# Optimization experiments

Measured on AMD Instinct MI355X. Metric: run time of the kernel, lower is better.

The kernel has to match this reference:

```python
import jax, jax.numpy as jnp
import numpy as np

D_MODEL = 1024
N_HEADS = 16
D_K = D_MODEL // N_HEADS


def setup_inputs() -> dict:
    key = jax.random.key(0)
    ks = jax.random.split(key, 11)
    B, S = 2, 2048
    scale = 0.02
    inp = {
        "q": jax.random.normal(ks[0], (B, S, D_MODEL), jnp.float32),
        "k": jax.random.normal(ks[1], (B, S, D_MODEL), jnp.float32),
        "v": jax.random.normal(ks[2], (B, S, D_MODEL), jnp.float32),
        "w_q": jax.random.normal(ks[3], (D_MODEL, D_MODEL), jnp.float32) * scale,
        "b_q": jnp.zeros((D_MODEL,), jnp.float32),
        "w_k": jax.random.normal(ks[4], (D_MODEL, D_MODEL), jnp.float32) * scale,
        "b_k": jnp.zeros((D_MODEL,), jnp.float32),
        "w_v": jax.random.normal(ks[5], (D_MODEL, D_MODEL), jnp.float32) * scale,
        "b_v": jnp.zeros((D_MODEL,), jnp.float32),
        "w_o": jax.random.normal(ks[6], (D_MODEL, D_MODEL), jnp.float32) * scale,
        "b_o": jnp.zeros((D_MODEL,), jnp.float32),
    }
    return inp


def reference(q, k, v, w_q, b_q, w_k, b_k, w_v, b_v, w_o, b_o):
    B, S, _ = q.shape
    # projections (torch Linear: x @ W.T + b); split into heads -> [B, H, S, d]
    def proj(x, w, b):
        return (x @ w.T + b).reshape(B, S, N_HEADS, D_K).transpose(0, 2, 1, 3)
    qh = proj(q, w_q, b_q)
    kh = proj(k, w_k, b_k)
    vh = proj(v, w_v, b_v)
    scores = jnp.einsum("bhqd,bhkd->bhqk", qh, kh) / jnp.sqrt(
        jnp.asarray(D_K, jnp.float32))
    attn = jax.nn.softmax(scores, axis=-1)  # dropout = identity (eval)
    out = jnp.einsum("bhqk,bhkd->bhqd", attn, vh)
    out = out.transpose(0, 2, 1, 3).reshape(B, S, D_MODEL)
    return out @ w_o.T + b_o
```

## Files before the change

kernel.cpp:

```cpp
#include <hip/hip_runtime.h>

typedef unsigned short u16;
typedef unsigned int u32;
typedef __attribute__((ext_vector_type(4))) unsigned short u16x4;
typedef __attribute__((ext_vector_type(8))) unsigned short u16x8;
typedef __attribute__((ext_vector_type(8))) __bf16 bf16x8;
typedef __attribute__((ext_vector_type(4))) float f32x4;

#define SEQ 2048
#define DMODEL 1024
#define LDP 3072
#define MM (DMODEL * DMODEL)

__device__ __forceinline__ u16 f2bf(float f) {
  unsigned u = __builtin_bit_cast(unsigned, f);
  u = (u + 0x7fffu + ((u >> 16) & 1u)) >> 16;
  return (u16)u;
}

__device__ __forceinline__ u32 cvtpk(float lo, float hi) {
  u32 r;
  asm volatile("v_cvt_pk_bf16_f32 %0, %1, %2" : "=v"(r) : "v"(lo), "v"(hi));
  return r;
}

__device__ __forceinline__ float fexp2(float x) {
#if __has_builtin(__builtin_amdgcn_exp2f)
  return __builtin_amdgcn_exp2f(x);
#else
  return exp2f(x);
#endif
}

__device__ __forceinline__ bf16x8 ldbf8(const u16* p) {
  return __builtin_bit_cast(bf16x8, *(const u16x8*)p);
}
__device__ __forceinline__ bf16x8 ldbf8c(const char* p) {
  return __builtin_bit_cast(bf16x8, *(const u16x8*)p);
}

__device__ __forceinline__ f32x4 mfma16(bf16x8 a, bf16x8 b, f32x4 c) {
  return __builtin_amdgcn_mfma_f32_16x16x32_bf16(a, b, c, 0, 0, 0);
}

__device__ __forceinline__ void gl16(const void* g, void* l) {
  __builtin_amdgcn_global_load_lds(
      (__attribute__((address_space(1))) void*)(size_t)g,
      (__attribute__((address_space(3))) void*)l, 16, 0, 0);
}

__device__ __forceinline__ void cast8(const float* __restrict__ s, u16* __restrict__ d) {
  const size_t i = ((size_t)blockIdx.x * blockDim.x + threadIdx.x) * 8;
  const float4 a = *(const float4*)(s + i);
  const float4 b = *(const float4*)(s + i + 4);
  u16x8 o;
  o[0] = f2bf(a.x); o[1] = f2bf(a.y); o[2] = f2bf(a.z); o[3] = f2bf(a.w);
  o[4] = f2bf(b.x); o[5] = f2bf(b.y); o[6] = f2bf(b.z); o[7] = f2bf(b.w);
  *(u16x8*)(d + i) = o;
}

__global__ void cast_qkv_k(const float* __restrict__ q, const float* __restrict__ k,
                           const float* __restrict__ v, u16* __restrict__ dq,
                           u16* __restrict__ dk, u16* __restrict__ dv) {
  const int z = blockIdx.y;
  cast8(z == 0 ? q : z == 1 ? k : v, z == 0 ? dq : z == 1 ? dk : dv);
}

__global__ void cast_w_k(const float* __restrict__ wq, const float* __restrict__ wk,
                         const float* __restrict__ wv, const float* __restrict__ wo,
                         u16* __restrict__ wqkv, u16* __restrict__ wob) {
  const int z = blockIdx.y;
  const float* s = z == 0 ? wq : z == 1 ? wk : z == 2 ? wv : wo;
  u16* d = z < 3 ? wqkv + (size_t)z * MM : wob;
  cast8(s, d);
}

template <int OMODE>
__device__ __forceinline__ void gemm_bt_body(const u16* __restrict__ A,
                                             const u16* __restrict__ Bw,
                                             const float* __restrict__ bias,
                                             void* __restrict__ Cv, const int K,
                                             const int ldc, const int ncol0,
                                             const int m0, const int n0) {
  __shared__ u16 As[128 * 32];
  __shared__ u16 Bs[128 * 32];
  const int tid = threadIdx.x;
  const int lane = tid & 63;
  const int w = tid >> 6;
  const int l15 = lane & 15;
  const int lg = lane >> 4;

  f32x4 acc[4][4] = {};

  const int arow = (w >> 1) * 64 + l15;
  const int brow = (w & 1) * 64 + l15;
  const int kfb = lg * 16;

  const int strow = w * 32 + (lane >> 2);
  const u16* Ag = A + (size_t)(m0 + strow) * K + (lane & 3) * 8;
  const u16* Bg = Bw + (size_t)(n0 + strow) * K + (lane & 3) * 8;
  const size_t rstep = (size_t)16 * K;
  char* AsL0 = (char*)As + w * 32 * 64;
  char* AsL1 = AsL0 + 16 * 64;
  char* BsL0 = (char*)Bs + w * 32 * 64;
  char* BsL1 = BsL0 + 16 * 64;

  for (int k0 = 0; k0 < K; k0 += 32) {
    __syncthreads();
    gl16(Ag + k0, AsL0);
    gl16(Ag + k0 + rstep, AsL1);
    gl16(Bg + k0, BsL0);
    gl16(Bg + k0 + rstep, BsL1);
    __syncthreads();
    bf16x8 af[4], bfv[4];
#pragma unroll
    for (int t = 0; t < 4; ++t) {
      af[t] = ldbf8c((char*)As + (arow + t * 16) * 64 + kfb);
      bfv[t] = ldbf8c((char*)Bs + (brow + t * 16) * 64 + kfb);
    }
    __builtin_amdgcn_s_setprio(1);
#pragma unroll
    for (int i = 0; i < 4; ++i)
#pragma unroll
      for (int j = 0; j < 4; ++j) acc[i][j] = mfma16(af[i], bfv[j], acc[i][j]);
    __builtin_amdgcn_s_setprio(0);
  }

  const int mrow = (w >> 1) * 64 + lg * 4;
  const int ncol = (w & 1) * 64 + l15;
#pragma unroll
  for (int j = 0; j < 4; ++j) {
    const int gn = n0 + ncol + j * 16;
    const float bia = bias[gn];
#pragma unroll
    for (int i = 0; i < 4; ++i) {
      const int gmb = m0 + mrow + i * 16;
#pragma unroll
      for (int r = 0; r < 4; ++r) {
        const float val = acc[i][j][r] + bia;
        const int gm = gmb + r;
        if (OMODE == 0) {
          ((float*)Cv)[(size_t)gm * ldc + gn] = val;
        } else if (OMODE == 1) {
          ((u16*)Cv)[(size_t)gm * ldc + ncol0 + gn] = f2bf(val);
        } else {
          const int bb = gm >> 11, ss = gm & 2047;
          const int hh = gn >> 6, dd = gn & 63;
          ((u16*)Cv)[(((size_t)(bb * 16 + hh) * 64 + dd) << 11) + ss] = f2bf(val);
        }
      }
    }
  }
}

__global__ __launch_bounds__(256, 3) void gemm_qkv_k(
    const u16* __restrict__ qb, const u16* __restrict__ kb,
    const u16* __restrict__ vb, const u16* __restrict__ wqkv,
    const float* __restrict__ bq, const float* __restrict__ bk,
    const float* __restrict__ bv, u16* __restrict__ proj, u16* __restrict__ vtb) {
  const int b = blockIdx.x;
  const int xcd = b & 7;
  const int i = b >> 3;
  const int z = i >> 5;
  const int j = i & 31;
  const int m0 = (xcd * 4 + (j >> 3)) * 128;
  const int n0 = (j & 7) * 128;
  if (z == 2)
    gemm_bt_body<2>(vb, wqkv + 2 * (size_t)MM, bv, vtb, DMODEL, 0, 0, m0, n0);
  else
    gemm_bt_body<1>(z == 0 ? qb : kb, wqkv + (size_t)z * MM, z == 0 ? bq : bk,
                    proj, DMODEL, LDP, z * DMODEL, m0, n0);
}

__global__ __launch_bounds__(256, 3) void gemm_o_k(const u16* __restrict__ attnb,
                                                   const u16* __restrict__ wob,
                                                   const float* __restrict__ bo,
                                                   float* __restrict__ out) {
  const int b = blockIdx.x;
  const int xcd = b & 7;
  const int i = b >> 3;
  const int m0 = (xcd * 4 + (i >> 3)) * 128;
  const int n0 = (i & 7) * 128;
  gemm_bt_body<0>(attnb, wob, bo, out, DMODEL, DMODEL, 0, m0, n0);
}

__global__ __launch_bounds__(256, 4) void attn_k(const u16* __restrict__ proj,
                                                 const u16* __restrict__ vtb,
                                                 u16* __restrict__ outa) {
  __shared__ u16 ks[2][64 * 64];
  __shared__ u16 vs[2][64 * 64];
  const int b = blockIdx.x;
  const int slot = b >> 3;
  const int bh = (b & 7) * 4 + (slot >> 5);
  const int qB = (slot & 31) * 64;
  const int tid = threadIdx.x;
  const int lane = tid & 63;
  const int w = tid >> 6;
  const size_t rb = (size_t)(bh >> 4) * SEQ;
  const int h = bh & 15;
  const int l15 = lane & 15;
  const int lg = lane >> 4;
  const int sw = (l15 & 7) << 4;
  const int c0 = (lg * 16) ^ sw;
  const int c1 = (lg * 16 + 64) ^ sw;
  const int rowb = l15 * 128;

  const u16* qp = proj + (rb + qB + w * 16 + l15) * LDP + h * 64 + lg * 8;
  const bf16x8 qf0 = ldbf8(qp);
  const bf16x8 qf1 = ldbf8(qp + 32);

  const int srow = tid >> 2;
  const int scel = (tid & 3) * 16;
  const int stz0 = srow * 128 + (((tid & 3) * 32) ^ ((srow & 7) << 4));
  const int stz1 = srow * 128 + ((((tid & 3) * 32) + 16) ^ ((srow & 7) << 4));
  const u16* kg = proj + rb * LDP + DMODEL + h * 64;
  const u16* vg = vtb + (size_t)bh * 64 * SEQ;

  u16x8 ka0, ka1, va0, va1;
  {
    const u16* kr = kg + (size_t)srow * LDP + scel;
    ka0 = *(const u16x8*)kr;
    ka1 = *(const u16x8*)(kr + 8);
    const u16* vr = vg + (size_t)srow * SEQ + scel;
    va0 = *(const u16x8*)vr;
    va1 = *(const u16x8*)(vr + 8);
  }

  f32x4 oacc[4] = {};
  float mrun = -3.0e38f, lrun = 0.f;
  int p = 0;

  for (int kv0 = 0; kv0 < SEQ; kv0 += 64) {
    {
      char* kd = (char*)ks[p];
      char* vd = (char*)vs[p];
      *(u16x8*)(kd + stz0) = ka0;
      *(u16x8*)(kd + stz1) = ka1;
      *(u16x8*)(vd + stz0) = va0;
      *(u16x8*)(vd + stz1) = va1;
    }
    __syncthreads();
    if (kv0 + 64 < SEQ) {
      const u16* kr = kg + (size_t)(kv0 + 64 + srow) * LDP + scel;
      ka0 = *(const u16x8*)kr;
      ka1 = *(const u16x8*)(kr + 8);
      const u16* vr = vg + (size_t)srow * SEQ + kv0 + 64 + scel;
      va0 = *(const u16x8*)vr;
      va1 = *(const u16x8*)(vr + 8);
    }
    const char* kb = (const char*)ks[p];
    f32x4 st[4];
    __builtin_amdgcn_s_setprio(1);
#pragma unroll
    for (int t = 0; t < 4; ++t) {
      const bf16x8 k0 = ldbf8c(kb + t * 2048 + rowb + c0);
      const bf16x8 k1 = ldbf8c(kb + t * 2048 + rowb + c1);
      f32x4 s = {};
      s = mfma16(k0, qf0, s);
      s = mfma16(k1, qf1, s);
      st[t] = s * 0.18033688f;
    }
    __builtin_amdgcn_s_setprio(0);

    float mx0 = fmaxf(fmaxf(st[0][0], st[0][1]), fmaxf(st[0][2], st[0][3]));
    float mx1 = fmaxf(fmaxf(st[1][0], st[1][1]), fmaxf(st[1][2], st[1][3]));
    float mx2 = fmaxf(fmaxf(st[2][0], st[2][1]), fmaxf(st[2][2], st[2][3]));
    float mx3 = fmaxf(fmaxf(st[3][0], st[3][1]), fmaxf(st[3][2], st[3][3]));
    float mx = fmaxf(fmaxf(mx0, mx1), fmaxf(mx2, mx3));
    mx = fmaxf(mx, __shfl_xor(mx, 16));
    mx = fmaxf(mx, __shfl_xor(mx, 32));
    if (!__all(mx <= mrun + 11.5416f)) {
      const float mn = fmaxf(mrun, mx);
      const float sf = fexp2(mrun - mn);
      mrun = mn;
      lrun *= sf;
#pragma unroll
      for (int t = 0; t < 4; ++t)
#pragma unroll
        for (int r = 0; r < 4; ++r) oacc[t][r] *= sf;
    }
    float rs = 0.f;
    u32 pku[4][2];
#pragma unroll
    for (int t = 0; t < 4; ++t) {
      const float e0 = fexp2(st[t][0] - mrun);
      const float e1 = fexp2(st[t][1] - mrun);
      const float e2 = fexp2(st[t][2] - mrun);
      const float e3 = fexp2(st[t][3] - mrun);
      rs += (e0 + e1) + (e2 + e3);
      pku[t][0] = cvtpk(e0, e1);
      pku[t][1] = cvtpk(e2, e3);
    }
    rs += __shfl_xor(rs, 16);
    rs += __shfl_xor(rs, 32);
    lrun += rs;

    u16x8 pb0, pb1;
    ((u32*)&pb0)[0] = pku[0][0]; ((u32*)&pb0)[1] = pku[0][1];
    ((u32*)&pb0)[2] = pku[1][0]; ((u32*)&pb0)[3] = pku[1][1];
    ((u32*)&pb1)[0] = pku[2][0]; ((u32*)&pb1)[1] = pku[2][1];
    ((u32*)&pb1)[2] = pku[3][0]; ((u32*)&pb1)[3] = pku[3][1];
    const bf16x8 pf0 = __builtin_bit_cast(bf16x8, pb0);
    const bf16x8 pf1 = __builtin_bit_cast(bf16x8, pb1);

    const char* vbp = (const char*)vs[p];
    const int vo0 = (8 * lg) ^ sw;
    __builtin_amdgcn_s_setprio(1);
#pragma unroll
    for (int dt = 0; dt < 4; ++dt) {
      const char* vrow = vbp + (dt * 16 + l15) * 128;
      u16x8 vf0, vf1;
      *(u16x4*)&vf0       = *(const u16x4*)(vrow + vo0);
      *((u16x4*)&vf0 + 1) = *(const u16x4*)(vrow + (vo0 ^ 32));
      *(u16x4*)&vf1       = *(const u16x4*)(vrow + (vo0 ^ 64));
      *((u16x4*)&vf1 + 1) = *(const u16x4*)(vrow + (vo0 ^ 96));
      oacc[dt] = mfma16(__builtin_bit_cast(bf16x8, vf0), pf0, oacc[dt]);
      oacc[dt] = mfma16(__builtin_bit_cast(bf16x8, vf1), pf1, oacc[dt]);
    }
    __builtin_amdgcn_s_setprio(0);
    p ^= 1;
  }

  const float invl = 1.0f / lrun;
  u16* orow = outa + (rb + qB + w * 16 + l15) * DMODEL + h * 64;
#pragma unroll
  for (int t = 0; t < 4; ++t) {
    const u32 p01 = cvtpk(oacc[t][0] * invl, oacc[t][1] * invl);
    const u32 p23 = cvtpk(oacc[t][2] * invl, oacc[t][3] * invl);
    *(u32*)((char*)orow + (t * 16 + lg * 4) * 2) = p01;
    *(u32*)((char*)orow + (t * 16 + lg * 4 + 2) * 2) = p23;
  }
}

extern "C" void kernel_launch(void* const* d_in, const int* in_sizes, int n_in,
                              void* d_out, int out_size, void* d_ws, size_t ws_size,
                              hipStream_t stream) {
  const float* q  = (const float*)d_in[0];
  const float* k  = (const float*)d_in[1];
  const float* v  = (const float*)d_in[2];
  const float* wq = (const float*)d_in[3];
  const float* bq = (const float*)d_in[4];
  const float* wk = (const float*)d_in[5];
  const float* bk = (const float*)d_in[6];
  const float* wv = (const float*)d_in[7];
  const float* bv = (const float*)d_in[8];
  const float* wo = (const float*)d_in[9];
  const float* bo = (const float*)d_in[10];

  const size_t NTOK = (size_t)2 * SEQ;
  const size_t NELE = NTOK * DMODEL;
  u16* qb    = (u16*)d_ws;
  u16* kb    = qb + NELE;
  u16* vb    = kb + NELE;
  u16* wqkv  = vb + NELE;
  u16* wob   = wqkv + 3 * (size_t)MM;
  u16* projb = wob + (size_t)MM;
  u16* vtb   = projb + NTOK * LDP;
  u16* attnb = qb;

  cast_qkv_k<<<dim3(2048, 3), 256, 0, stream>>>(q, k, v, qb, kb, vb);
  cast_w_k<<<dim3(512, 4), 256, 0, stream>>>(wq, wk, wv, wo, wqkv, wob);
  gemm_qkv_k<<<768, 256, 0, stream>>>(qb, kb, vb, wqkv, bq, bk, bv, projb, vtb);
  attn_k<<<1024, 256, 0, stream>>>(projb, vtb, attnb);
  gemm_o_k<<<256, 256, 0, stream>>>(attnb, wob, bo, (float*)d_out);
}
```

Before: 141.7 us.

## Switch attention to 32x32x16 MFMA with 128-query tiles per block

The attention kernel now has each wave handle 32 query rows with 32x32x16 bf16 MFMAs instead of 16 rows with 16x16x32. Each block covers 128 queries, which halves the grid and halves K/V LDS staging traffic per query. The softmax scale is folded into an FMA inside exp2, and the rescale threshold is adjusted to match unscaled scores. The trade is more accumulator registers (launch bounds drop from 4 to 2 blocks per CU) and fewer blocks, which lowers occupancy and parallelism.

After: 127.3 us. -10.1%, faster.

```diff
diff --git a/kernel.cpp b/kernel.cpp
--- a/kernel.cpp
+++ b/kernel.cpp
@@ -6,11 +6,13 @@
 typedef __attribute__((ext_vector_type(8))) unsigned short u16x8;
 typedef __attribute__((ext_vector_type(8))) __bf16 bf16x8;
 typedef __attribute__((ext_vector_type(4))) float f32x4;
+typedef __attribute__((ext_vector_type(16))) float f32x16;
 
 #define SEQ 2048
 #define DMODEL 1024
 #define LDP 3072
 #define MM (DMODEL * DMODEL)
+#define SC 0.18033688f
 
 __device__ __forceinline__ u16 f2bf(float f) {
   unsigned u = __builtin_bit_cast(unsigned, f);
@@ -41,6 +43,9 @@
 
 __device__ __forceinline__ f32x4 mfma16(bf16x8 a, bf16x8 b, f32x4 c) {
   return __builtin_amdgcn_mfma_f32_16x16x32_bf16(a, b, c, 0, 0, 0);
+}
+__device__ __forceinline__ f32x16 mfma32(bf16x8 a, bf16x8 b, f32x16 c) {
+  return __builtin_amdgcn_mfma_f32_32x32x16_bf16(a, b, c, 0, 0, 0);
 }
 
 __device__ __forceinline__ void gl16(const void* g, void* l) {
@@ -184,30 +189,28 @@
   gemm_bt_body<0>(attnb, wob, bo, out, DMODEL, DMODEL, 0, m0, n0);
 }
 
-__global__ __launch_bounds__(256, 4) void attn_k(const u16* __restrict__ proj,
+__global__ __launch_bounds__(256, 2) void attn_k(const u16* __restrict__ proj,
                                                  const u16* __restrict__ vtb,
                                                  u16* __restrict__ outa) {
   __shared__ u16 ks[2][64 * 64];
   __shared__ u16 vs[2][64 * 64];
   const int b = blockIdx.x;
   const int slot = b >> 3;
-  const int bh = (b & 7) * 4 + (slot >> 5);
-  const int qB = (slot & 31) * 64;
+  const int bh = (b & 7) * 4 + (slot >> 4);
+  const int qB = (slot & 15) * 128;
   const int tid = threadIdx.x;
   const int lane = tid & 63;
   const int w = tid >> 6;
   const size_t rb = (size_t)(bh >> 4) * SEQ;
   const int h = bh & 15;
-  const int l15 = lane & 15;
-  const int lg = lane >> 4;
-  const int sw = (l15 & 7) << 4;
-  const int c0 = (lg * 16) ^ sw;
-  const int c1 = (lg * 16 + 64) ^ sw;
-  const int rowb = l15 * 128;
-
-  const u16* qp = proj + (rb + qB + w * 16 + l15) * LDP + h * 64 + lg * 8;
-  const bf16x8 qf0 = ldbf8(qp);
-  const bf16x8 qf1 = ldbf8(qp + 32);
+  const int l31 = lane & 31;
+  const int hi = lane >> 5;
+  const int swz = (l31 & 7) << 4;
+
+  const u16* qp = proj + (rb + qB + w * 32 + l31) * LDP + h * 64 + hi * 8;
+  bf16x8 qf[4];
+#pragma unroll
+  for (int km = 0; km < 4; ++km) qf[km] = ldbf8(qp + km * 16);
 
   const int srow = tid >> 2;
   const int scel = (tid & 3) * 16;
@@ -226,7 +229,7 @@
     va1 = *(const u16x8*)(vr + 8);
   }
 
-  f32x4 oacc[4] = {};
+  f32x16 oa0 = {}, oa1 = {};
   float mrun = -3.0e38f, lrun = 0.f;
   int p = 0;
 
@@ -248,87 +251,96 @@
       va0 = *(const u16x8*)vr;
       va1 = *(const u16x8*)(vr + 8);
     }
-    const char* kb = (const char*)ks[p];
-    f32x4 st[4];
+    const char* kp = (const char*)ks[p];
+    const char* vp = (const char*)vs[p];
+    f32x16 s0 = {}, s1 = {};
     __builtin_amdgcn_s_setprio(1);
 #pragma unroll
-    for (int t = 0; t < 4; ++t) {
-      const bf16x8 k0 = ldbf8c(kb + t * 2048 + rowb + c0);
-      const bf16x8 k1 = ldbf8c(kb + t * 2048 + rowb + c1);
-      f32x4 s = {};
-      s = mfma16(k0, qf0, s);
-      s = mfma16(k1, qf1, s);
-      st[t] = s * 0.18033688f;
+    for (int km = 0; km < 4; ++km) {
+      const int co = (km * 32 + hi * 16) ^ swz;
+      const bf16x8 k0 = ldbf8c(kp + l31 * 128 + co);
+      const bf16x8 k1 = ldbf8c(kp + (32 + l31) * 128 + co);
+      s0 = mfma32(k0, qf[km], s0);
+      s1 = mfma32(k1, qf[km], s1);
     }
     __builtin_amdgcn_s_setprio(0);
 
-    float mx0 = fmaxf(fmaxf(st[0][0], st[0][1]), fmaxf(st[0][2], st[0][3]));
-    float mx1 = fmaxf(fmaxf(st[1][0], st[1][1]), fmaxf(st[1][2], st[1][3]));
-    float mx2 = fmaxf(fmaxf(st[2][0], st[2][1]), fmaxf(st[2][2], st[2][3]));
-    float mx3 = fmaxf(fmaxf(st[3][0], st[3][1]), fmaxf(st[3][2], st[3][3]));
-    float mx = fmaxf(fmaxf(mx0, mx1), fmaxf(mx2, mx3));
-    mx = fmaxf(mx, __shfl_xor(mx, 16));
+    float mxq0 = fmaxf(fmaxf(s0[0], s0[1]), fmaxf(s0[2], s0[3]));
+    float mxq1 = fmaxf(fmaxf(s0[4], s0[5]), fmaxf(s0[6], s0[7]));
+    float mxq2 = fmaxf(fmaxf(s0[8], s0[9]), fmaxf(s0[10], s0[11]));
+    float mxq3 = fmaxf(fmaxf(s0[12], s0[13]), fmaxf(s0[14], s0[15]));
+    float mxq4 = fmaxf(fmaxf(s1[0], s1[1]), fmaxf(s1[2], s1[3]));
+    float mxq5 = fmaxf(fmaxf(s1[4], s1[5]), fmaxf(s1[6], s1[7]));
+    float mxq6 = fmaxf(fmaxf(s1[8], s1[9]), fmaxf(s1[10], s1[11]));
+    float mxq7 = fmaxf(fmaxf(s1[12], s1[13]), fmaxf(s1[14], s1[15]));
+    float mx = fmaxf(fmaxf(fmaxf(mxq0, mxq1), fmaxf(mxq2, mxq3)),
+                     fmaxf(fmaxf(mxq4, mxq5), fmaxf(mxq6, mxq7)));
     mx = fmaxf(mx, __shfl_xor(mx, 32));
-    if (!__all(mx <= mrun + 11.5416f)) {
+    if (!__all(mx <= mrun + 64.0f)) {
       const float mn = fmaxf(mrun, mx);
-      const float sf = fexp2(mrun - mn);
+      const float sf = fexp2((mrun - mn) * SC);
       mrun = mn;
       lrun *= sf;
 #pragma unroll
-      for (int t = 0; t < 4; ++t)
-#pragma unroll
-        for (int r = 0; r < 4; ++r) oacc[t][r] *= sf;
-    }
-    float rs = 0.f;
-    u32 pku[4][2];
-#pragma unroll
-    for (int t = 0; t < 4; ++t) {
-      const float e0 = fexp2(st[t][0] - mrun);
-      const float e1 = fexp2(st[t][1] - mrun);
-      const float e2 = fexp2(st[t][2] - mrun);
-      const float e3 = fexp2(st[t][3] - mrun);
-      rs += (e0 + e1) + (e2 + e3);
-      pku[t][0] = cvtpk(e0, e1);
-      pku[t][1] = cvtpk(e2, e3);
-    }
-    rs += __shfl_xor(rs, 16);
+      for (int r = 0; r < 16; ++r) { oa0[r] *= sf; oa1[r] *= sf; }
+    }
+    const float nmc = -mrun * SC;
+#pragma unroll
+    for (int r = 0; r < 16; ++r) s0[r] = fexp2(__builtin_fmaf(s0[r], SC, nmc));
+#pragma unroll
+    for (int r = 0; r < 16; ++r) s1[r] = fexp2(__builtin_fmaf(s1[r], SC, nmc));
+    float rs = (((s0[0] + s0[1]) + (s0[2] + s0[3])) +
+                ((s0[4] + s0[5]) + (s0[6] + s0[7]))) +
+               (((s0[8] + s0[9]) + (s0[10] + s0[11])) +
+                ((s0[12] + s0[13]) + (s0[14] + s0[15])));
+    rs += (((s1[0] + s1[1]) + (s1[2] + s1[3])) +
+           ((s1[4] + s1[5]) + (s1[6] + s1[7]))) +
+          (((s1[8] + s1[9]) + (s1[10] + s1[11])) +
+           ((s1[12] + s1[13]) + (s1[14] + s1[15])));
     rs += __shfl_xor(rs, 32);
     lrun += rs;
 
-    u16x8 pb0, pb1;
-    ((u32*)&pb0)[0] = pku[0][0]; ((u32*)&pb0)[1] = pku[0][1];
-    ((u32*)&pb0)[2] = pku[1][0]; ((u32*)&pb0)[3] = pku[1][1];
-    ((u32*)&pb1)[0] = pku[2][0]; ((u32*)&pb1)[1] = pku[2][1];
-    ((u32*)&pb1)[2] = pku[3][0]; ((u32*)&pb1)[3] = pku[3][1];
-    const bf16x8 pf0 = __builtin_bit_cast(bf16x8, pb0);
-    const bf16x8 pf1 = __builtin_bit_cast(bf16x8, pb1);
-
-    const char* vbp = (const char*)vs[p];
-    const int vo0 = (8 * lg) ^ sw;
     __builtin_amdgcn_s_setprio(1);
-#pragma unroll
-    for (int dt = 0; dt < 4; ++dt) {
-      const char* vrow = vbp + (dt * 16 + l15) * 128;
-      u16x8 vf0, vf1;
-      *(u16x4*)&vf0       = *(const u16x4*)(vrow + vo0);
-      *((u16x4*)&vf0 + 1) = *(const u16x4*)(vrow + (vo0 ^ 32));
-      *(u16x4*)&vf1       = *(const u16x4*)(vrow + (vo0 ^ 64));
-      *((u16x4*)&vf1 + 1) = *(const u16x4*)(vrow + (vo0 ^ 96));
-      oacc[dt] = mfma16(__builtin_bit_cast(bf16x8, vf0), pf0, oacc[dt]);
-      oacc[dt] = mfma16(__builtin_bit_cast(bf16x8, vf1), pf1, oacc[dt]);
-    }
+#define PCHUNK(SV, G, CB)                                                \
+    {                                                                    \
+      u16x8 pbu;                                                         \
+      ((u32*)&pbu)[0] = cvtpk(SV[G + 0], SV[G + 1]);                     \
+      ((u32*)&pbu)[1] = cvtpk(SV[G + 2], SV[G + 3]);                     \
+      ((u32*)&pbu)[2] = cvtpk(SV[G + 4], SV[G + 5]);                     \
+      ((u32*)&pbu)[3] = cvtpk(SV[G + 6], SV[G + 7]);                     \
+      const bf16x8 pb = __builtin_bit_cast(bf16x8, pbu);                 \
+      const int vc0 = (CB + 8 * hi) ^ swz;                               \
+      const int vc1 = (CB + 16 + 8 * hi) ^ swz;                          \
+      const char* vr0 = vp + l31 * 128;                                  \
+      const char* vr1 = vp + (32 + l31) * 128;                           \
+      u16x8 vf0, vf1;                                                    \
+      *(u16x4*)&vf0       = *(const u16x4*)(vr0 + vc0);                  \
+      *((u16x4*)&vf0 + 1) = *(const u16x4*)(vr0 + vc1);                  \
+      *(u16x4*)&vf1       = *(const u16x4*)(vr1 + vc0);                  \
+      *((u16x4*)&vf1 + 1) = *(const u16x4*)(vr1 + vc1);                  \
+      oa0 = mfma32(__builtin_bit_cast(bf16x8, vf0), pb, oa0);            \
+      oa1 = mfma32(__builtin_bit_cast(bf16x8, vf1), pb, oa1);            \
+    }
+    PCHUNK(s0, 0, 0)
+    PCHUNK(s0, 8, 32)
+    PCHUNK(s1, 0, 64)
+    PCHUNK(s1, 8, 96)
+#undef PCHUNK
     __builtin_amdgcn_s_setprio(0);
     p ^= 1;
   }
 
   const float invl = 1.0f / lrun;
-  u16* orow = outa + (rb + qB + w * 16 + l15) * DMODEL + h * 64;
-#pragma unroll
-  for (int t = 0; t < 4; ++t) {
-    const u32 p01 = cvtpk(oacc[t][0] * invl, oacc[t][1] * invl);
-    const u32 p23 = cvtpk(oacc[t][2] * invl, oacc[t][3] * invl);
-    *(u32*)((char*)orow + (t * 16 + lg * 4) * 2) = p01;
-    *(u32*)((char*)orow + (t * 16 + lg * 4 + 2) * 2) = p23;
+  u16* orow = outa + (rb + qB + w * 32 + l31) * DMODEL + h * 64 + hi * 4;
+#pragma unroll
+  for (int g = 0; g < 4; ++g) {
+    u16x4 st0, st1;
+    ((u32*)&st0)[0] = cvtpk(oa0[4 * g + 0] * invl, oa0[4 * g + 1] * invl);
+    ((u32*)&st0)[1] = cvtpk(oa0[4 * g + 2] * invl, oa0[4 * g + 3] * invl);
+    *(u16x4*)(orow + 8 * g) = st0;
+    ((u32*)&st1)[0] = cvtpk(oa1[4 * g + 0] * invl, oa1[4 * g + 1] * invl);
+    ((u32*)&st1)[1] = cvtpk(oa1[4 * g + 2] * invl, oa1[4 * g + 3] * invl);
+    *(u16x4*)(orow + 32 + 8 * g) = st1;
   }
 }
 
@@ -361,6 +373,6 @@
   cast_qkv_k<<<dim3(2048, 3), 256, 0, stream>>>(q, k, v, qb, kb, vb);
   cast_w_k<<<dim3(512, 4), 256, 0, stream>>>(wq, wk, wv, wo, wqkv, wob);
   gemm_qkv_k<<<768, 256, 0, stream>>>(qb, kb, vb, wqkv, bq, bk, bv, projb, vtb);
-  attn_k<<<1024, 256, 0, stream>>>(projb, vtb, attnb);
+  attn_k<<<512, 256, 0, stream>>>(projb, vtb, attnb);
   gemm_o_k<<<256, 256, 0, stream>>>(attnb, wob, bo, (float*)d_out);
 }
```
